# Performance work log

Measured on AMD Instinct MI355X. Metric: run time of the kernel, lower is better.

The kernel has to match this reference:

```python
import jax, jax.numpy as jnp
import numpy as np

B, Hh, Ww, C = 8, 64, 64, 384
Dg = C // 2          # 192, per-group d_model
Di = Dg              # expand=1 -> d_inner = d_model
K = 2                # scan directions per group
S = 1                # d_state
R = -(-Dg // 16)     # dt_rank = ceil(d_model/16) = 12
Cout = 384


def setup_inputs() -> dict:
    key = jax.random.key(0)
    ks = jax.random.split(key, 30)
    n = lambda k, shp, s=0.05: (jax.random.normal(k, shp, jnp.float32) * s)
    inp = {
        "x": jax.random.normal(ks[0], (B, Hh * Ww, C), jnp.float32),
        "norm_g": jnp.ones((C,), jnp.float32),
        "norm_b": jnp.zeros((C,), jnp.float32),
        # DynamicChannelSorter (reduction=2)
        "r_w1": n(ks[1], (C // 2, C)), "r_b1": n(ks[2], (C // 2,)),
        "r_w2": n(ks[3], (C, C // 2)), "r_b2": n(ks[4], (C,)),
        # SS2D params stacked over 2 groups
        "in_proj_w": n(ks[5], (2, 2 * Di, Dg)),
        "conv_w": n(ks[6], (2, Di, 1, 3, 3), 0.1),
        "conv_b": n(ks[7], (2, Di), 0.02),
        "x_proj_w": n(ks[8], (2, K, R + 2 * S, Di)),
        "dt_proj_w": n(ks[9], (2, K, Di, R), 0.1),
        "dt_proj_b": n(ks[10], (2, K, Di), 0.5) - 3.0,   # softplus-inv of small dt
        "A_log": n(ks[11], (2, K, Di, S), 0.1),
        "Ds": jnp.ones((2, K, Di), jnp.float32),
        "out_norm_g": jnp.ones((2, Di), jnp.float32),
        "out_norm_b": jnp.zeros((2, Di), jnp.float32),
        "out_proj_w": n(ks[12], (2, Dg, Di)),
        # channel_interaction (reduction=16)
        "ci_w1": n(ks[13], (C // 16, C)), "ci_b1": n(ks[14], (C // 16,)),
        "ci_w2": n(ks[15], (C, C // 16)), "ci_b2": n(ks[16], (C,)),
        "proj_w": n(ks[17], (Cout, C)), "proj_b": n(ks[18], (Cout,)),
        "skip_scale": jnp.ones((1,), jnp.float32),
        "H": Hh, "W": Ww,
    }
    return inp


def _ln(x, g, b, eps=1e-5):
    m = x.mean(-1, keepdims=True)
    v = jnp.mean((x - m) ** 2, -1, keepdims=True)
    return (x - m) * jax.lax.rsqrt(v + eps) * g + b


def _selective_scan(xs, dts, Bm, Cm, A, D):
    # xs,dts: (B,K,Di,L); Bm,Cm: (B,K,S,L); A: (K,Di,S); D: (K,Di)
    dA = jnp.exp(dts[..., None] * A[None, :, :, None, :])              # (B,K,Di,L,S)
    dBx = dts[..., None] * jnp.swapaxes(Bm, -1, -2)[:, :, None] * xs[..., None]
    dA_t = jnp.moveaxis(dA, 3, 0)                                      # (L,B,K,Di,S)
    dBx_t = jnp.moveaxis(dBx, 3, 0)
    C_t = jnp.moveaxis(Cm, -1, 0)                                      # (L,B,K,S)
    h0 = jnp.zeros(dA.shape[:3] + (dA.shape[-1],), xs.dtype)           # (B,K,Di,S)

    def step(h, inp):
        a, bx, c = inp
        h = a * h + bx
        return h, jnp.einsum('bkcs,bks->bkc', h, c)

    _, ys = jax.lax.scan(step, h0, (dA_t, dBx_t, C_t))                 # (L,B,K,Di)
    ys = jnp.moveaxis(ys, 0, -1)                                       # (B,K,Di,L)
    return ys + D[None, :, :, None] * xs


def _ss2d(x, in_w, cw, cb, xp_w, dt_w, dt_b, A_log, D, on_g, on_b, op_w, vertical):
    # x: (B,H,W,Dg). VMamba-style SS2D with K=2 directions.
    b, h, w, _ = x.shape
    L = h * w
    xz = jnp.einsum('bhwc,dc->bhwd', x, in_w)                          # (B,H,W,2*Di)
    xc, z = jnp.split(xz, 2, axis=-1)
    xc = jnp.transpose(xc, (0, 3, 1, 2))                               # (B,Di,H,W)
    xc = jax.lax.conv_general_dilated(
        xc, cw, (1, 1), 'SAME', feature_group_count=Di,
        dimension_numbers=('NCHW', 'OIHW', 'NCHW')) + cb[None, :, None, None]
    xc = jax.nn.silu(xc)
    xf = jnp.transpose(xc, (0, 1, 3, 2)) if vertical else xc
    xflat = xf.reshape(b, Di, L)
    xs = jnp.stack([xflat, jnp.flip(xflat, -1)], axis=1)               # (B,K,Di,L)
    x_dbl = jnp.einsum('bkcl,kdc->bkdl', xs, xp_w)
    r = dt_w.shape[-1]
    dts, Bm, Cm = x_dbl[:, :, :r], x_dbl[:, :, r:r + S], x_dbl[:, :, r + S:r + 2 * S]
    dts = jax.nn.softplus(jnp.einsum('bkrl,kdr->bkdl', dts, dt_w) + dt_b[None, :, :, None])
    A = -jnp.exp(A_log)
    ys = _selective_scan(xs, dts, Bm, Cm, A, D)                        # (B,K,Di,L)
    y = ys[:, 0] + jnp.flip(ys[:, 1], -1)                              # cross-merge
    if vertical:
        y = jnp.transpose(y.reshape(b, Di, w, h), (0, 1, 3, 2))
    else:
        y = y.reshape(b, Di, h, w)
    y = jnp.transpose(y, (0, 2, 3, 1))                                 # (B,H,W,Di)
    y = _ln(y, on_g, on_b)
    y = y * jax.nn.silu(z)
    return jnp.einsum('bhwd,od->bhwo', y, op_w)


def reference(x, norm_g, norm_b, r_w1, r_b1, r_w2, r_b2, in_proj_w, conv_w,
              conv_b, x_proj_w, dt_proj_w, dt_proj_b, A_log, Ds, out_norm_g,
              out_norm_b, out_proj_w, ci_w1, ci_b1, ci_w2, ci_b2, proj_w,
              proj_b, skip_scale, H, W):
    b, n, c = x.shape
    residual = x
    xn = _ln(x, norm_g, norm_b)
    # dynamic channel sorter
    pool = xn.mean(axis=1)                                             # (B,C)
    scores = jax.nn.sigmoid(jax.nn.relu(pool @ r_w1.T + r_b1) @ r_w2.T + r_b2)
    sort_idx = jnp.argsort(-scores, axis=1)
    inv_idx = jnp.argsort(sort_idx, axis=1)
    x_sorted = jnp.take_along_axis(xn, sort_idx[:, None, :], axis=2)
    xsp = x_sorted.reshape(b, H, W, c)
    x1, x2 = jnp.split(xsp, 2, axis=-1)
    y1 = _ss2d(x1, in_proj_w[0], conv_w[0], conv_b[0], x_proj_w[0], dt_proj_w[0],
               dt_proj_b[0], A_log[0], Ds[0], out_norm_g[0], out_norm_b[0],
               out_proj_w[0], vertical=False)
    y2 = _ss2d(x2, in_proj_w[1], conv_w[1], conv_b[1], x_proj_w[1], dt_proj_w[1],
               dt_proj_b[1], A_log[1], Ds[1], out_norm_g[1], out_norm_b[1],
               out_proj_w[1], vertical=True)
    y_cat = jnp.concatenate([y1, y2], axis=-1).reshape(b, n, c)
    y_restored = jnp.take_along_axis(y_cat, inv_idx[:, None, :], axis=2)
    gate = jax.nn.sigmoid(jax.nn.relu(xn @ ci_w1.T + ci_b1) @ ci_w2.T + ci_b2)
    y_final = (y_restored * gate) @ proj_w.T + proj_b
    return residual + y_final * skip_scale
```

## Files before the change

### kernel.cpp

```cpp
#include <hip/hip_runtime.h>
#include <math.h>

#define NB 8
#define LTOK 4096
#define CH 384
#define DH 192
#define HH 64
#define WW 64
#define NCHK 128
#define CHS 32

static constexpr long BLC  = (long)NB * LTOK * CH;
static constexpr long CST  = (long)32 * NCHK * DH;

typedef unsigned short u16;
typedef u16   u16x8 __attribute__((ext_vector_type(8)));
typedef short s16x8 __attribute__((ext_vector_type(8)));
typedef float f32x4 __attribute__((ext_vector_type(4)));

__device__ inline u16 f2bf(float f){
  unsigned int u = __float_as_uint(f);
  return (u16)((u + 0x7FFFu + ((u >> 16) & 1u)) >> 16);
}
__device__ inline float bf2f(u16 h){ return __uint_as_float(((unsigned int)h) << 16); }
__device__ inline float fsigmoid(float x){ return 1.f / (1.f + __expf(-x)); }
__device__ inline unsigned cvt_pk_bf16(float lo, float hi){
  unsigned r;
  asm("v_cvt_pk_bf16_f32 %0, %1, %2" : "=v"(r) : "v"(lo), "v"(hi));
  return r;
}
__device__ inline void gl16(const u16* g, u16* l){
  __builtin_amdgcn_global_load_lds(
      (const __attribute__((address_space(1))) void*)g,
      (__attribute__((address_space(3))) void*)l, 16, 0, 0);
}

#define SCOL(ml, c) ((c) ^ ((((ml) >> 2) & 3) << 4))

template<int NW>
__device__ inline float blockSum(float v, float* sm){
  #pragma unroll
  for (int o = 32; o > 0; o >>= 1) v += __shfl_down(v, o);
  int lane = threadIdx.x & 63, wv = threadIdx.x >> 6;
  if (lane == 0) sm[wv] = v;
  __syncthreads();
  if (threadIdx.x == 0){ float t = 0.f; for (int i = 0; i < NW; i++) t += sm[i]; sm[0] = t; }
  __syncthreads();
  float t = sm[0];
  __syncthreads();
  return t;
}

__global__ __launch_bounds__(128) void k_ln(const float* __restrict__ x,
    const float* __restrict__ g, const float* __restrict__ b, float* __restrict__ xn){
  __shared__ float sm[2];
  long row = blockIdx.x;
  int t = threadIdx.x;
  const float* xr = x + row * CH;
  float v0 = xr[t], v1 = xr[t + 128], v2 = xr[t + 256];
  float s = blockSum<2>(v0 + v1 + v2, sm);
  float m = s * (1.f / CH);
  float d0 = v0 - m, d1 = v1 - m, d2 = v2 - m;
  float vs = blockSum<2>(d0*d0 + d1*d1 + d2*d2, sm);
  float inv = rsqrtf(vs * (1.f / CH) + 1e-5f);
  float* o = xn + row * CH;
  o[t]       = d0 * inv * g[t]       + b[t];
  o[t + 128] = d1 * inv * g[t + 128] + b[t + 128];
  o[t + 256] = d2 * inv * g[t + 256] + b[t + 256];
}

__global__ __launch_bounds__(128) void k_pool(const float* __restrict__ xn, float* __restrict__ pp){
  int c = blockIdx.x * 128 + threadIdx.x;
  int chunk = blockIdx.y, b = blockIdx.z;
  long base = ((long)b * LTOK + chunk * 256) * CH;
  float s = 0.f;
  for (int n = 0; n < 256; n++) s += xn[base + (long)n * CH + c];
  pp[((long)b * 16 + chunk) * CH + c] = s;
}

__global__ __launch_bounds__(384) void k_score(const float* __restrict__ pp,
    const float* __restrict__ w1, const float* __restrict__ b1,
    const float* __restrict__ w2, const float* __restrict__ b2,
    int* __restrict__ sidx, int* __restrict__ inv){
  __shared__ float poolv[CH];
  __shared__ float hid[192];
  __shared__ float sc[CH];
  int b = blockIdx.x, t = threadIdx.x;
  float s = 0.f;
  for (int ch = 0; ch < 16; ch++) s += pp[((long)b * 16 + ch) * CH + t];
  poolv[t] = s * (1.f / LTOK);
  __syncthreads();
  if (t < 192){
    float h = b1[t];
    for (int c = 0; c < CH; c++) h += poolv[c] * w1[t * CH + c];
    hid[t] = fmaxf(h, 0.f);
  }
  __syncthreads();
  {
    float h = b2[t];
    for (int j = 0; j < 192; j++) h += hid[j] * w2[t * 192 + j];
    sc[t] = 1.f / (1.f + expf(-h));
  }
  __syncthreads();
  float mys = sc[t];
  int rank = 0;
  for (int j = 0; j < CH; j++){
    float o = sc[j];
    rank += (o > mys) || (o == mys && j < t);
  }
  sidx[b * CH + rank] = t;
  inv[b * CH + t] = rank;
}

__global__ __launch_bounds__(256) void k_preps(const float* __restrict__ in_proj,
    const float* __restrict__ op_w, const float* __restrict__ proj_w,
    const float* __restrict__ alog, const float* __restrict__ cw,
    u16* __restrict__ wip, u16* __restrict__ wop, u16* __restrict__ wpj,
    float* __restrict__ Atab, u16* __restrict__ cwb){
  const int N1 = 2*384*192;
  const int N2 = N1 + 2*192*192;
  const int N3 = N2 + 384*384;
  const int N4 = N3 + 4*192;
  const int N5 = N4 + 2*9*DH;
  int i = blockIdx.x * 256 + threadIdx.x;
  if (i < N1)      wip[i] = f2bf(in_proj[i]);
  else if (i < N2) wop[i-N1] = f2bf(op_w[i-N1]);
  else if (i < N3) wpj[i-N2] = f2bf(proj_w[i-N2]);
  else if (i < N4) Atab[i-N3] = -expf(alog[i-N3]);
  else if (i < N5){
    int r = i - N4;
    int g = r / (9*DH); int r2 = r - g*9*DH;
    int tap = r2 / DH, di = r2 - tap*DH;
    cwb[r] = f2bf(cw[((long)g*DH + di)*9 + tap]);
  }
}

__global__ __launch_bounds__(384) void k_castgather(const float* __restrict__ xn,
    const int* __restrict__ sidx, u16* __restrict__ As){
  long row = blockIdx.x;
  int b = (int)(row >> 12);
  int t = threadIdx.x;
  int c = sidx[b * CH + t];
  As[row * CH + t] = f2bf(xn[row * CH + c]);
}

__global__ __launch_bounds__(256) void k_prepw(const float* __restrict__ w1,
    const float* __restrict__ b1, const float* __restrict__ w2,
    const int* __restrict__ sidx, u16* __restrict__ w1g, u16* __restrict__ w2p,
    float* __restrict__ b1p){
  int b = blockIdx.x, tid = threadIdx.x;
  if (b < NB){
    const int* sx = sidx + b * CH;
    for (int i = tid; i < 32 * CH; i += 256){
      int j = i / CH, r = i - j * CH;
      float v = (j < 24) ? w1[j * CH + sx[r]] : 0.f;
      w1g[(long)b * 32 * CH + i] = f2bf(v);
    }
  } else {
    for (int i = tid; i < CH * 32; i += 256){
      int n = i >> 5, j = i & 31;
      w2p[i] = f2bf((j < 24) ? w2[n * 24 + j] : 0.f);
    }
    if (tid < 32) b1p[tid] = (tid < 24) ? b1[tid] : 0.f;
  }
}

__global__ __launch_bounds__(256) void k_prepM(const float* __restrict__ dtw,
    const float* __restrict__ xpw, u16* __restrict__ Mw){
  int gk = blockIdx.y;
  int g = gk >> 1, k = gk & 1;
  int idx = blockIdx.x * 256 + threadIdx.x;
  int di = idx / 192, c = idx - di * 192;
  float s = 0.f;
  #pragma unroll
  for (int r = 0; r < 12; r++)
    s += dtw[((long)gk * 192 + di) * 12 + r] * xpw[(long)g * 5376 + (k * 14 + r) * 192 + c];
  Mw[(long)gk * 36864 + idx] = f2bf(s);
}

__global__ __launch_bounds__(256) void k_hid(const u16* __restrict__ As,
    const u16* __restrict__ w1g, const float* __restrict__ b1p,
    u16* __restrict__ hidp){
  __shared__ u16 sA[128 * 32];
  __shared__ u16 sB[32 * 32];
  int b = blockIdx.y;
  const u16* Ab = As + (long)b * LTOK * CH;
  const u16* Bb = w1g + (long)b * 32 * CH;
  int tid = threadIdx.x;
  int m0 = blockIdx.x * 128;
  int wv = tid >> 6, l = tid & 63;
  int wm = wv * 32;
  int kg = l >> 4, lr = l & 15;

  f32x4 acc[2][2];
  #pragma unroll
  for (int i = 0; i < 2; i++)
    #pragma unroll
    for (int j = 0; j < 2; j++)
      #pragma unroll
      for (int r = 0; r < 4; r++) acc[i][j][r] = 0.f;

  int aoffU[2], boffU[2];
  #pragma unroll
  for (int i = 0; i < 2; i++){
    int r = wm + i * 16 + lr;
    aoffU[i] = r * 32 + ((kg * 8) ^ ((r & 3) << 3));
  }
  #pragma unroll
  for (int j = 0; j < 2; j++){
    int r = j * 16 + lr;
    boffU[j] = r * 32 + ((kg * 8) ^ ((r & 3) << 3));
  }

  u16x8 ra[2], rbv;
  #pragma unroll
  for (int q = 0; q < 2; q++){
    int i = q * 256 + tid; int row = i >> 2, sl = i & 3, ss = sl ^ (row & 3);
    ra[q] = *(const u16x8*)(Ab + (long)(m0 + row) * CH + ss * 8);
  }
  if (tid < 128){
    int row = tid >> 2, sl = tid & 3, ss = sl ^ (row & 3);
    rbv = *(const u16x8*)(Bb + (long)row * CH + ss * 8);
  }

  const int nks = CH / 32;
  for (int ks = 0; ks < nks; ks++){
    __syncthreads();
    #pragma unroll
    for (int q = 0; q < 2; q++){
      int i = q * 256 + tid; int row = i >> 2, sl = i & 3;
      *(u16x8*)(sA + row * 32 + sl * 8) = ra[q];
    }
    if (tid < 128){
      int row = tid >> 2, sl = tid & 3;
      *(u16x8*)(sB + row * 32 + sl * 8) = rbv;
    }
    __syncthreads();
    if (ks + 1 < nks){
      int k0 = (ks + 1) * 32;
      #pragma unroll
      for (int q = 0; q < 2; q++){
        int i = q * 256 + tid; int row = i >> 2, sl = i & 3, ss = sl ^ (row & 3);
        ra[q] = *(const u16x8*)(Ab + (long)(m0 + row) * CH + k0 + ss * 8);
      }
      if (tid < 128){
        int row = tid >> 2, sl = tid & 3, ss = sl ^ (row & 3);
        rbv = *(const u16x8*)(Bb + (long)row * CH + k0 + ss * 8);
      }
    }
    s16x8 af[2], bfr[2];
    #pragma unroll
    for (int i = 0; i < 2; i++) af[i] = *(const s16x8*)(sA + aoffU[i]);
    #pragma unroll
    for (int j = 0; j < 2; j++) bfr[j] = *(const s16x8*)(sB + boffU[j]);
    #pragma unroll
    for (int i = 0; i < 2; i++)
      #pragma unroll
      for (int j = 0; j < 2; j++)
        acc[i][j] = __builtin_amdgcn_mfma_f32_16x16x32_bf16(af[i], bfr[j], acc[i][j], 0, 0, 0);
  }

  #pragma unroll
  for (int i = 0; i < 2; i++)
    #pragma unroll
    for (int j = 0; j < 2; j++)
      #pragma unroll
      for (int r = 0; r < 4; r++){
        int m = m0 + wm + i * 16 + kg * 4 + r;
        int n = j * 16 + lr;
        float v = fmaxf(acc[i][j][r] + b1p[n], 0.f);
        hidp[((long)b * LTOK + m) * 32 + n] = f2bf(v);
      }
}

template<int BN, int MODE>
__global__ __launch_bounds__(256) void k_mm(
    const u16* __restrict__ A, int lda, long aOuter, long aInner,
    const u16* __restrict__ B, long bInner,
    float* __restrict__ Cf, u16* __restrict__ Ch,
    long cOuter, long cInner, int ldc,
    int K, int innerCnt,
    const float* __restrict__ bias, const float* __restrict__ resid,
    const float* __restrict__ skip,
    const u16* __restrict__ gy, const int* __restrict__ ginv){
  constexpr int BM = 128;
  constexpr int AI = 2;
  constexpr int BI = (BN * 32) / (256 * 8);
  constexpr int NJ = BN / 32;
  __shared__ u16 sA[BM * 32];
  __shared__ u16 sB[BN * 32];

  int bz = blockIdx.z;
  int bo = bz / innerCnt, bi_ = bz - bo * innerCnt;
  const u16* Ab = A + (long)bo * aOuter + (long)bi_ * aInner;
  const u16* Bb = B + (long)bi_ * bInner;
  int tid = threadIdx.x;
  int m0 = blockIdx.y * BM, n0 = blockIdx.x * BN;
  int wv = tid >> 6, l = tid & 63;
  int wm = (wv >> 1) * 64, wn = (wv & 1) * (BN / 2);
  int kg = l >> 4, lr = l & 15;

  f32x4 acc[4][NJ];
  #pragma unroll
  for (int i = 0; i < 4; i++)
    #pragma unroll
    for (int j = 0; j < NJ; j++)
      #pragma unroll
      for (int r = 0; r < 4; r++) acc[i][j][r] = 0.f;

  int aoffU[4], boffU[NJ];
  #pragma unroll
  for (int i = 0; i < 4; i++){
    int r = wm + i * 16 + lr;
    aoffU[i] = r * 32 + ((kg * 8) ^ ((r & 3) << 3));
  }
  #pragma unroll
  for (int j = 0; j < NJ; j++){
    int r = wn + j * 16 + lr;
    boffU[j] = r * 32 + ((kg * 8) ^ ((r & 3) << 3));
  }

  int wb = tid & 192;
  int nks = K >> 5;
  for (int ks = 0; ks < nks; ks++){
    int k0 = ks << 5;
    __syncthreads();
    #pragma unroll
    for (int q = 0; q < AI; q++){
      int i = q * 256 + tid; int row = i >> 2, ss = (i & 3) ^ (row & 3);
      gl16(Ab + (long)(m0 + row) * lda + k0 + ss * 8, sA + (q * 256 + wb) * 8);
    }
    #pragma unroll
    for (int q = 0; q < BI; q++){
      int i = q * 256 + tid; int row = i >> 2, ss = (i & 3) ^ (row & 3);
      gl16(Bb + (long)(n0 + row) * K + k0 + ss * 8, sB + (q * 256 + wb) * 8);
    }
    __syncthreads();
    s16x8 af[4];
    #pragma unroll
    for (int i = 0; i < 4; i++) af[i] = *(const s16x8*)(sA + aoffU[i]);
    s16x8 bfr[NJ];
    #pragma unroll
    for (int j = 0; j < NJ; j++) bfr[j] = *(const s16x8*)(sB + boffU[j]);
    #pragma unroll
    for (int i = 0; i < 4; i++)
      #pragma unroll
      for (int j = 0; j < NJ; j++)
        acc[i][j] = __builtin_amdgcn_mfma_f32_16x16x32_bf16(af[i], bfr[j], acc[i][j], 0, 0, 0);
  }

  long zc = (long)bo * cOuter + (long)bi_ * cInner;
  #pragma unroll
  for (int i = 0; i < 4; i++){
    #pragma unroll
    for (int j = 0; j < NJ; j++){
      #pragma unroll
      for (int r = 0; r < 4; r++){
        int m = m0 + wm + i * 16 + kg * 4 + r;
        int n = n0 + wn + j * 16 + lr;
        float v = acc[i][j][r];
        if constexpr (MODE == 1){
          if (n < 192) ((u16*)Cf)[zc + (long)m * 192 + n] = f2bf(v);
          else         Ch[zc + (long)m * 192 + (n - 192)] = f2bf(v * fsigmoid(v));
        } else if constexpr (MODE == 2){
          Ch[zc + (long)m * ldc + n] = f2bf(v);
        } else if constexpr (MODE == 3){
          float vb = v + bias[n];
          long o = (long)m * ldc + n;
          Cf[o] = resid[o] + skip[0] * vb;
        } else {
          float gate = fsigmoid(v + bias[n]);
          int bt = m >> 12;
          float yr = bf2f(gy[(long)m * ldc + ginv[bt * CH + n]]);
          Ch[(long)m * ldc + n] = f2bf(yr * gate);
        }
      }
    }
  }
}

__global__ __launch_bounds__(256) void k_dt(
    const u16* __restrict__ xcvh, const u16* __restrict__ Mw,
    const float* __restrict__ dtb, const float* __restrict__ Atab,
    const float* __restrict__ bc, u16* __restrict__ pk16,
    float* __restrict__ cP, float* __restrict__ cS){
  constexpr int NJ = 2;
  __shared__ unsigned sMem[64 * 64];
  u16* sA = (u16*)sMem;
  u16* sB = (u16*)(sMem + 1024);

  int z = blockIdx.z;
  int bg = z >> 1, kk_ = z & 1, g = bg & 1, gk = g * 2 + kk_;
  const u16* Ab = xcvh + (long)bg * LTOK * 192;
  const u16* Bb = Mw + (long)gk * 36864;
  int tid = threadIdx.x;
  int m0 = blockIdx.y * 64, n0 = blockIdx.x * 64;
  int wv = tid >> 6, l = tid & 63;
  int wm = (wv >> 1) * 32, wn = (wv & 1) * 32;
  int kg = l >> 4, lr = l & 15;

  f32x4 acc[2][NJ];
  #pragma unroll
  for (int i = 0; i < 2; i++)
    #pragma unroll
    for (int j = 0; j < NJ; j++)
      #pragma unroll
      for (int r = 0; r < 4; r++) acc[i][j][r] = 0.f;

  int aoffU[2], boffU[NJ];
  #pragma unroll
  for (int i = 0; i < 2; i++){
    int r = wm + i * 16 + lr;
    aoffU[i] = r * 32 + ((kg * 8) ^ ((r & 3) << 3));
  }
  #pragma unroll
  for (int j = 0; j < NJ; j++){
    int r = wn + j * 16 + lr;
    boffU[j] = r * 32 + ((kg * 8) ^ ((r & 3) << 3));
  }

  int srow = tid >> 2, sss = (tid & 3) ^ (srow & 3);
  int wb = tid & 192;
  const int nks = 6;
  for (int ks = 0; ks < nks; ks++){
    int k0 = ks << 5;
    __syncthreads();
    gl16(Ab + (long)(m0 + srow) * 192 + k0 + sss * 8, sA + wb * 8);
    gl16(Bb + (long)(n0 + srow) * 192 + k0 + sss * 8, sB + wb * 8);
    __syncthreads();
    s16x8 af[2], bfr[NJ];
    #pragma unroll
    for (int i = 0; i < 2; i++) af[i] = *(const s16x8*)(sA + aoffU[i]);
    #pragma unroll
    for (int j = 0; j < NJ; j++) bfr[j] = *(const s16x8*)(sB + boffU[j]);
    #pragma unroll
    for (int i = 0; i < 2; i++)
      #pragma unroll
      for (int j = 0; j < NJ; j++)
        acc[i][j] = __builtin_amdgcn_mfma_f32_16x16x32_bf16(af[i], bfr[j], acc[i][j], 0, 0, 0);
  }

  unsigned pkreg[2][NJ][4];
  float dtbj[NJ], Atlj[NJ];
  #pragma unroll
  for (int j = 0; j < NJ; j++){
    int n = n0 + wn + j * 16 + lr;
    dtbj[j] = dtb[gk * 192 + n];
    Atlj[j] = Atab[gk * 192 + n];
  }
  #pragma unroll
  for (int i = 0; i < 2; i++){
    #pragma unroll
    for (int r = 0; r < 4; r++){
      int ml = wm + i * 16 + kg * 4 + r;
      int m = m0 + ml;
      long rowz = (long)z * LTOK + m;
      long rowx = (long)bg * LTOK + m;
      float Bv = bc[rowz * 2];
      float dts[NJ];
      #pragma unroll
      for (int j = 0; j < NJ; j++){
        float rr = acc[i][j][r] + dtbj[j];
        float dtv = __logf(1.f + __expf(rr));
        float av  = __expf(Atlj[j] * dtv);
        float xv  = bf2f(xcvh[rowx * 192 + n0 + wn + j * 16 + lr]);
        dts[j] = dtv;
        pkreg[i][j][r] = cvt_pk_bf16(av, dtv * Bv * xv);
      }
      unsigned dtp = cvt_pk_bf16(dts[0], dts[1]);
      pk16[rowz * 192 + n0 + wn + lr]      = (u16)(dtp & 0xFFFFu);
      pk16[rowz * 192 + n0 + wn + 16 + lr] = (u16)(dtp >> 16);
    }
  }

  __syncthreads();
  #pragma unroll
  for (int i = 0; i < 2; i++){
    #pragma unroll
    for (int j = 0; j < NJ; j++){
      #pragma unroll
      for (int r = 0; r < 4; r++){
        int ml = wm + i * 16 + kg * 4 + r;
        int cl = wn + j * 16 + lr;
        sMem[ml * 64 + SCOL(ml, cl)] = pkreg[i][j][r];
      }
    }
  }
  __syncthreads();

  if (tid < 128){
    int cc = tid >> 6, nn = tid & 63;
    float P = 1.f, S = 0.f;
    if (kk_ == 0){
      for (int s = 0; s < CHS; s++){
        int row = cc * CHS + s;
        unsigned v = sMem[row * 64 + SCOL(row, nn)];
        float a = bf2f((u16)(v & 0xFFFFu));
        float dBx = bf2f((u16)(v >> 16));
        P *= a; S = a * S + dBx;
      }
    } else {
      for (int s = CHS - 1; s >= 0; s--){
        int row = cc * CHS + s;
        unsigned v = sMem[row * 64 + SCOL(row, nn)];
        float a = bf2f((u16)(v & 0xFFFFu));
        float dBx = bf2f((u16)(v >> 16));
        P *= a; S = a * S + dBx;
      }
    }
    int cglob = (kk_ == 0) ? (blockIdx.y * 2 + cc)
                           : (NCHK - 1 - blockIdx.y * 2 - cc);
    long idx = ((long)z * NCHK + cglob) * 192 + n0 + nn;
    cP[idx] = P;
    cS[idx] = S;
  }
}

__global__ __launch_bounds__(192) void k_conv(const u16* __restrict__ xch,
    const u16* __restrict__ cwb, const float* __restrict__ cb,
    const float* __restrict__ xpw, u16* __restrict__ xcvh,
    float* __restrict__ bc){
  __shared__ float red[8][4][25];
  int tid = threadIdx.x;
  int chg = tid % 24, pp = tid / 24;
  int p = blockIdx.x * 8 + pp;
  int bg = blockIdx.y; int g = bg & 1;
  int h = p >> 6, w = p & 63;
  int di = chg * 8;
  long sb = (long)bg * LTOK;

  u16x8 wv[9];
  #pragma unroll
  for (int t = 0; t < 9; t++)
    wv[t] = *(const u16x8*)(cwb + ((long)g * 9 + t) * DH + di);

  float acc[8];
  #pragma unroll
  for (int j = 0; j < 8; j++) acc[j] = cb[g * DH + di + j];

  #pragma unroll
  for (int dh = -1; dh <= 1; dh++){
    int hh = h + dh; if (hh < 0 || hh >= HH) continue;
    #pragma unroll
    for (int dw = -1; dw <= 1; dw++){
      int ww2 = w + dw; if (ww2 < 0 || ww2 >= WW) continue;
      u16x8 xv = *(const u16x8*)(xch + (sb + hh * WW + ww2) * DH + di);
      int t = (dh + 1) * 3 + (dw + 1);
      #pragma unroll
      for (int j = 0; j < 8; j++) acc[j] += bf2f(wv[t][j]) * bf2f(xv[j]);
    }
  }

  u16x8 ov;
  #pragma unroll
  for (int j = 0; j < 8; j++){
    float s = acc[j];
    acc[j] = s * fsigmoid(s);
    ov[j] = f2bf(acc[j]);
  }
  int lscan = (g == 0) ? p : (w * HH + h);
  *(u16x8*)(xcvh + (sb + lscan) * DH + di) = ov;

  #pragma unroll
  for (int j = 0; j < 4; j++){
    int k = j >> 1, ci = j & 1;
    const float* wl = xpw + (long)g * 5376 + (k * 14 + 12 + ci) * 192 + di;
    float sacc = 0.f;
    #pragma unroll
    for (int q = 0; q < 8; q++) sacc += acc[q] * wl[q];
    red[pp][j][chg] = sacc;
  }
  __syncthreads();
  if (tid < 32){
    int pos = tid >> 2, j = tid & 3;
    float ssum = 0.f;
    #pragma unroll
    for (int q = 0; q < 24; q++) ssum += red[pos][j][q];
    int p2 = blockIdx.x * 8 + pos;
    int h2 = p2 >> 6, w2 = p2 & 63;
    int ls = (g == 0) ? p2 : (w2 * HH + h2);
    int k = j >> 1;
    bc[(((long)(bg * 2 + k)) * LTOK + ls) * 2 + (j & 1)] = ssum;
  }
}

__global__ __launch_bounds__(192) void k_scan_p2(const float* __restrict__ cP,
    const float* __restrict__ cS, float* __restrict__ h0){
  int z = blockIdx.x;
  int di = threadIdx.x;
  float h = 0.f;
  for (int c = 0; c < NCHK; c++){
    long idx = ((long)z * NCHK + c) * 192 + di;
    h0[idx] = h;
    h = cP[idx] * h + cS[idx];
  }
}

__global__ __launch_bounds__(192) void k_scan_p3(const u16* __restrict__ pk16,
    const u16* __restrict__ xcvh, const float* __restrict__ bc,
    const float* __restrict__ Atab, const float* __restrict__ ds,
    const float* __restrict__ h0, const u16* __restrict__ zsh,
    const float* __restrict__ ong, const float* __restrict__ onb,
    u16* __restrict__ yab){
  __shared__ float yl[CHS][193];
  __shared__ float red[2][32][6];
  __shared__ float minv[2][32];
  int bg = blockIdx.x, c = blockIdx.y;
  int g = bg & 1;
  int di = threadIdx.x;
  const u16* xc = xcvh + (long)bg * LTOK * 192 + di;
  int l0 = c * CHS;
  float yv[CHS];

  {
    int z = bg * 2, gk = g * 2;
    float Dv = ds[gk * 192 + di], Av = Atab[gk * 192 + di];
    const u16* pk = pk16 + (long)z * LTOK * 192 + di;
    const float* bcp = bc + (long)z * LTOK * 2;
    float h = h0[((long)z * NCHK + c) * 192 + di];
    #pragma unroll
    for (int s = 0; s < CHS; s++){
      int l = l0 + s;
      float dtv = bf2f(pk[(long)l * 192]);
      float av  = __expf(Av * dtv);
      float xv  = bf2f(xc[(long)l * 192]);
      float Bv  = bcp[l * 2], Cv = bcp[l * 2 + 1];
      h = av * h + dtv * Bv * xv;
      yv[s] = h * Cv + Dv * xv;
    }
  }
  {
    int z = bg * 2 + 1, gk = g * 2 + 1;
    float Dv = ds[gk * 192 + di], Av = Atab[gk * 192 + di];
    const u16* pk = pk16 + (long)z * LTOK * 192 + di;
    const float* bcp = bc + (long)z * LTOK * 2;
    int cc = NCHK - 1 - c;
    float h = h0[((long)z * NCHK + cc) * 192 + di];
    #pragma unroll
    for (int s = CHS - 1; s >= 0; s--){
      int l = l0 + s;
      float dtv = bf2f(pk[(long)l * 192]);
      float av  = __expf(Av * dtv);
      float xv  = bf2f(xc[(long)l * 192]);
      float Bv  = bcp[l * 2], Cv = bcp[l * 2 + 1];
      h = av * h + dtv * Bv * xv;
      yv[s] += h * Cv + Dv * xv;
    }
  }

  #pragma unroll
  for (int s = 0; s < CHS; s++) yl[s][di] = yv[s];
  __syncthreads();
  {
    int pos = di & 31, seg = di >> 5;
    float s1 = 0.f, s2 = 0.f;
    #pragma unroll
    for (int q = 0; q < 32; q++){
      float v = yl[pos][seg * 32 + q];
      s1 += v; s2 += v * v;
    }
    red[0][pos][seg] = s1;
    red[1][pos][seg] = s2;
  }
  __syncthreads();
  if (di < 32){
    float s1 = 0.f, s2 = 0.f;
    #pragma unroll
    for (int q = 0; q < 6; q++){ s1 += red[0][di][q]; s2 += red[1][di][q]; }
    float m = s1 * (1.f / DH);
    float var = s2 * (1.f / DH) - m * m;
    minv[0][di] = m;
    minv[1][di] = rsqrtf(var + 1e-5f);
  }
  __syncthreads();

  float gng = ong[g * 192 + di], gnb = onb[g * 192 + di];
  long zbase = (long)bg * LTOK;
  #pragma unroll
  for (int s = 0; s < CHS; s++){
    int l = l0 + s;
    int p = (g == 0) ? l : ((l & 63) * 64 + (l >> 6));
    float m = minv[0][s], inv = minv[1][s];
    float yln = (yv[s] - m) * inv * gng + gnb;
    float zs = bf2f(zsh[(zbase + p) * 192 + di]);
    yab[(zbase + p) * 192 + di] = f2bf(yln * zs);
  }
}

extern "C" void kernel_launch(void* const* d_in, const int* in_sizes, int n_in,
                              void* d_out, int out_size, void* d_ws, size_t ws_size,
                              hipStream_t stream){
  const float* x       = (const float*)d_in[0];
  const float* norm_g  = (const float*)d_in[1];
  const float* norm_b  = (const float*)d_in[2];
  const float* r_w1    = (const float*)d_in[3];
  const float* r_b1    = (const float*)d_in[4];
  const float* r_w2    = (const float*)d_in[5];
  const float* r_b2    = (const float*)d_in[6];
  const float* in_proj = (const float*)d_in[7];
  const float* conv_w  = (const float*)d_in[8];
  const float* conv_b  = (const float*)d_in[9];
  const float* xp_w    = (const float*)d_in[10];
  const float* dt_w    = (const float*)d_in[11];
  const float* dt_b    = (const float*)d_in[12];
  const float* A_log   = (const float*)d_in[13];
  const float* Ds      = (const float*)d_in[14];
  const float* on_g    = (const float*)d_in[15];
  const float* on_b    = (const float*)d_in[16];
  const float* op_w    = (const float*)d_in[17];
  const float* ci_w1   = (const float*)d_in[18];
  const float* ci_b1   = (const float*)d_in[19];
  const float* ci_w2   = (const float*)d_in[20];
  const float* ci_b2   = (const float*)d_in[21];
  const float* proj_w  = (const float*)d_in[22];
  const float* proj_b  = (const float*)d_in[23];
  const float* skip    = (const float*)d_in[24];
  float* out = (float*)d_out;
  float* ws  = (float*)d_ws;

  float* xn   = ws;
  float* xcb  = ws + BLC;
  float* R3   = ws + 2 * BLC;
  float* R4   = R3 + BLC / 2;
  float* R5   = R4 + BLC / 2;
  float* pp   = R5 + BLC / 2;
  int*  sidx  = (int*)(pp + NB * 16 * CH);
  int*  inv   = sidx + NB * CH;
  u16*  wip   = (u16*)(inv + NB * CH);
  u16*  wop   = wip + 2 * 384 * 192;
  u16*  wpj   = wop + 2 * 192 * 192;
  u16*  w1g   = wpj + 384 * 384;
  u16*  w2p   = w1g + NB * 32 * CH;
  u16*  Mw    = w2p + CH * 32;
  u16*  cwb   = Mw + 4 * 192 * 192;
  float* b1p  = (float*)(cwb + 2 * 9 * DH);
  float* Atab = b1p + 32;
  u16*  hidp  = (u16*)(Atab + 4 * 192);
  float* bc   = (float*)(hidp + (long)NB * LTOK * 32);
  float* cP   = bc + 32 * LTOK * 2;
  float* cS   = cP + CST;
  float* h0   = cS + CST;

  size_t need = ((size_t)(2 * BLC) + 3 * (BLC / 2) + NB * 16 * CH + 32 * LTOK * 2 + 3 * CST + 64) * 4
              + (size_t)(2 * NB * CH) * 4 + (size_t)(4 * 192 + 32) * 4
              + ((size_t)2*384*192 + 2*192*192 + 384*384 + NB*32*CH + CH*32 + 4*192*192
                 + 2*9*DH + (size_t)NB * LTOK * 32) * 2
              + 8192;
  if (ws_size < need) return;

  u16*  As   = (u16*)R5;
  u16*  zsh  = (u16*)R3;
  u16*  xcbh = (u16*)xcb;
  u16*  xcvh = (u16*)R4;
  u16*  pk16 = (u16*)ws;
  u16*  yab  = (u16*)R5;
  u16*  ycat = (u16*)R3;
  u16*  gab  = (u16*)xcb;

  k_ln<<<NB * LTOK, 128, 0, stream>>>(x, norm_g, norm_b, xn);
  k_preps<<<1457, 256, 0, stream>>>(in_proj, op_w, proj_w, A_log, conv_w,
                                    wip, wop, wpj, Atab, cwb);
  k_prepM<<<dim3(144, 4), 256, 0, stream>>>(dt_w, xp_w, Mw);
  k_pool<<<dim3(3, 16, NB), 128, 0, stream>>>(xn, pp);
  k_score<<<NB, 384, 0, stream>>>(pp, r_w1, r_b1, r_w2, r_b2, sidx, inv);
  k_castgather<<<NB * LTOK, 384, 0, stream>>>(xn, sidx, As);
  k_prepw<<<NB + 1, 256, 0, stream>>>(ci_w1, ci_b1, ci_w2, sidx, w1g, w2p, b1p);

  k_mm<128, 1><<<dim3(3, 32, 16), 256, 0, stream>>>(
      As, CH, (long)LTOK * CH, 192,
      wip, (long)384 * 192,
      (float*)xcbh, zsh, (long)2 * LTOK * DH, (long)LTOK * DH, 0,
      192, 2, nullptr, nullptr, nullptr, nullptr, nullptr);

  k_hid<<<dim3(32, NB), 256, 0, stream>>>(As, w1g, b1p, hidp);

  k_conv<<<dim3(LTOK / 8, NB * 2), 192, 0, stream>>>(xcbh, cwb, conv_b, xp_w, xcvh, bc);

  k_dt<<<dim3(3, 64, 32), 256, 0, stream>>>(xcvh, Mw, dt_b, Atab, bc, pk16, cP, cS);

  k_scan_p2<<<32, 192, 0, stream>>>(cP, cS, h0);

  k_scan_p3<<<dim3(NB * 2, NCHK), 192, 0, stream>>>(
      pk16, xcvh, bc, Atab, Ds, h0, zsh, on_g, on_b, yab);

  k_mm<64, 2><<<dim3(3, 32, 16), 256, 0, stream>>>(
      yab, DH, (long)2 * LTOK * DH, (long)LTOK * DH,
      wop, (long)192 * 192,
      nullptr, ycat, (long)LTOK * CH, 192, CH,
      192, 2, nullptr, nullptr, nullptr, nullptr, nullptr);

  k_mm<128, 4><<<dim3(3, 256, 1), 256, 0, stream>>>(
      hidp, 32, 0, 0,
      w2p, 0,
      nullptr, gab, 0, 0, CH,
      32, 1, ci_b2, nullptr, nullptr, ycat, inv);

  k_mm<128, 3><<<dim3(3, 256, 1), 256, 0, stream>>>(
      gab, CH, 0, 0,
      wpj, 0,
      out, nullptr, 0, 0, CH,
      CH, 1, proj_b, x, skip, nullptr, nullptr);
}
```

Baseline: 364.2 us.

## Add 64x64-tile GEMM loading full 192-wide K slab for in/out/final projections

```diff
diff --git a/kernel.cpp b/kernel.cpp
--- a/kernel.cpp
+++ b/kernel.cpp
@@ -273,6 +273,102 @@
       }
 }
 
+template<int NITER, int MODE>
+__global__ __launch_bounds__(256) void k_mm2(
+    const u16* __restrict__ A, int lda, long aOuter, long aInner,
+    const u16* __restrict__ B, int ldb, long bInner,
+    float* __restrict__ Cf, u16* __restrict__ Ch,
+    long cOuter, long cInner, int ldc,
+    int innerCnt,
+    const float* __restrict__ bias, const float* __restrict__ resid,
+    const float* __restrict__ skip){
+  __shared__ u16 sA[64 * 192];
+  __shared__ u16 sB[64 * 192];
+
+  int bz = blockIdx.z;
+  int bo = bz / innerCnt, bi_ = bz - bo * innerCnt;
+  const u16* Ab = A + (long)bo * aOuter + (long)bi_ * aInner;
+  const u16* Bb = B + (long)bi_ * bInner;
+  int tid = threadIdx.x;
+  int m0 = blockIdx.y * 64, n0 = blockIdx.x * 64;
+  int wv = tid >> 6, l = tid & 63;
+  int wm = (wv >> 1) * 32, wn = (wv & 1) * 32;
+  int kg = l >> 4, lr = l & 15;
+  int wb = tid & 192;
+
+  f32x4 acc[2][2];
+  #pragma unroll
+  for (int i = 0; i < 2; i++)
+    #pragma unroll
+    for (int j = 0; j < 2; j++)
+      #pragma unroll
+      for (int r = 0; r < 4; r++) acc[i][j][r] = 0.f;
+
+  int koff = 0;
+  #pragma unroll
+  for (int kit = 0; kit < NITER; kit++, koff += 192){
+    if (kit > 0) __syncthreads();
+    #pragma unroll
+    for (int q = 0; q < 6; q++){
+      int p = q * 256 + tid;
+      int r = p / 24, sp = p - r * 24;
+      int sl = sp ^ (r & 7);
+      gl16(Ab + (long)(m0 + r) * lda + koff + sl * 8, sA + (q * 256 + wb) * 8);
+    }
+    #pragma unroll
+    for (int q = 0; q < 6; q++){
+      int p = q * 256 + tid;
+      int r = p / 24, sp = p - r * 24;
+      int sl = sp ^ (r & 7);
+      gl16(Bb + (long)(n0 + r) * ldb + koff + sl * 8, sB + (q * 256 + wb) * 8);
+    }
+    __syncthreads();
+    #pragma unroll
+    for (int ks = 0; ks < 6; ks++){
+      s16x8 af[2], bfr[2];
+      #pragma unroll
+      for (int i = 0; i < 2; i++){
+        int r = wm + i * 16 + lr;
+        af[i] = *(const s16x8*)(sA + r * 192 + (((ks * 4 + kg) ^ (r & 7)) * 8));
+      }
+      #pragma unroll
+      for (int j = 0; j < 2; j++){
+        int r = wn + j * 16 + lr;
+        bfr[j] = *(const s16x8*)(sB + r * 192 + (((ks * 4 + kg) ^ (r & 7)) * 8));
+      }
+      #pragma unroll
+      for (int i = 0; i < 2; i++)
+        #pragma unroll
+        for (int j = 0; j < 2; j++)
+          acc[i][j] = __builtin_amdgcn_mfma_f32_16x16x32_bf16(af[i], bfr[j], acc[i][j], 0, 0, 0);
+    }
+  }
+
+  long zc = (long)bo * cOuter + (long)bi_ * cInner;
+  #pragma unroll
+  for (int i = 0; i < 2; i++){
+    #pragma unroll
+    for (int j = 0; j < 2; j++){
+      #pragma unroll
+      for (int r = 0; r < 4; r++){
+        int m = m0 + wm + i * 16 + kg * 4 + r;
+        int n = n0 + wn + j * 16 + lr;
+        float v = acc[i][j][r];
+        if constexpr (MODE == 1){
+          if (n < 192) ((u16*)Cf)[zc + (long)m * 192 + n] = f2bf(v);
+          else         Ch[zc + (long)m * 192 + (n - 192)] = f2bf(v * fsigmoid(v));
+        } else if constexpr (MODE == 2){
+          Ch[zc + (long)m * ldc + n] = f2bf(v);
+        } else {
+          float vb = v + bias[n];
+          long o = (long)m * ldc + n;
+          Cf[o] = resid[o] + skip[0] * vb;
+        }
+      }
+    }
+  }
+}
+
 template<int BN, int MODE>
 __global__ __launch_bounds__(256) void k_mm(
     const u16* __restrict__ A, int lda, long aOuter, long aInner,
@@ -359,16 +455,7 @@
         int m = m0 + wm + i * 16 + kg * 4 + r;
         int n = n0 + wn + j * 16 + lr;
         float v = acc[i][j][r];
-        if constexpr (MODE == 1){
-          if (n < 192) ((u16*)Cf)[zc + (long)m * 192 + n] = f2bf(v);
-          else         Ch[zc + (long)m * 192 + (n - 192)] = f2bf(v * fsigmoid(v));
-        } else if constexpr (MODE == 2){
-          Ch[zc + (long)m * ldc + n] = f2bf(v);
-        } else if constexpr (MODE == 3){
-          float vb = v + bias[n];
-          long o = (long)m * ldc + n;
-          Cf[o] = resid[o] + skip[0] * vb;
-        } else {
+        if constexpr (MODE == 4){
           float gate = fsigmoid(v + bias[n]);
           int bt = m >> 12;
           float yr = bf2f(gy[(long)m * ldc + ginv[bt * CH + n]]);
@@ -766,11 +853,11 @@
   k_castgather<<<NB * LTOK, 384, 0, stream>>>(xn, sidx, As);
   k_prepw<<<NB + 1, 256, 0, stream>>>(ci_w1, ci_b1, ci_w2, sidx, w1g, w2p, b1p);
 
-  k_mm<128, 1><<<dim3(3, 32, 16), 256, 0, stream>>>(
+  k_mm2<1, 1><<<dim3(6, 64, 16), 256, 0, stream>>>(
       As, CH, (long)LTOK * CH, 192,
-      wip, (long)384 * 192,
+      wip, 192, (long)384 * 192,
       (float*)xcbh, zsh, (long)2 * LTOK * DH, (long)LTOK * DH, 0,
-      192, 2, nullptr, nullptr, nullptr, nullptr, nullptr);
+      2, nullptr, nullptr, nullptr);
 
   k_hid<<<dim3(32, NB), 256, 0, stream>>>(As, w1g, b1p, hidp);
 
@@ -783,11 +870,11 @@
   k_scan_p3<<<dim3(NB * 2, NCHK), 192, 0, stream>>>(
       pk16, xcvh, bc, Atab, Ds, h0, zsh, on_g, on_b, yab);
 
-  k_mm<64, 2><<<dim3(3, 32, 16), 256, 0, stream>>>(
+  k_mm2<1, 2><<<dim3(3, 64, 16), 256, 0, stream>>>(
       yab, DH, (long)2 * LTOK * DH, (long)LTOK * DH,
-      wop, (long)192 * 192,
+      wop, 192, (long)192 * 192,
       nullptr, ycat, (long)LTOK * CH, 192, CH,
-      192, 2, nullptr, nullptr, nullptr, nullptr, nullptr);
+      2, nullptr, nullptr, nullptr);
 
   k_mm<128, 4><<<dim3(3, 256, 1), 256, 0, stream>>>(
       hidp, 32, 0, 0,
@@ -795,9 +882,9 @@
       nullptr, gab, 0, 0, CH,
       32, 1, ci_b2, nullptr, nullptr, ycat, inv);
 
-  k_mm<128, 3><<<dim3(3, 256, 1), 256, 0, stream>>>(
+  k_mm2<2, 3><<<dim3(6, 512, 1), 256, 0, stream>>>(
       gab, CH, 0, 0,
-      wpj, 0,
+      wpj, 384, 0,
       out, nullptr, 0, 0, CH,
-      CH, 1, proj_b, x, skip, nullptr, nullptr);
-}
+      1, proj_b, x, skip);
+}
```

After: 352.4 us. -3.2%, faster.
